# Kernel tuning notes

Hardware: AMD Instinct MI355X
Metric: run time of the kernel (lower is better)

Reference implementation:

```python
import jax, jax.numpy as jnp
import numpy as np

BN_EPS = 1e-5

def _batchnorm(x):
    # BatchNorm1d(affine=False) in training mode: per-feature batch stats, biased var
    mu = jnp.mean(x, axis=0, keepdims=True)
    var = jnp.mean((x - mu) ** 2, axis=0, keepdims=True)
    return (x - mu) / jnp.sqrt(var + BN_EPS)

def setup_inputs() -> dict:
    key = jax.random.key(0)
    ks = jax.random.split(key, 8)
    H, I, S, E = 1024, 4096, 128, 16384  # hidden, intermediate, sqrt(experts), experts
    std = 0.02
    return {
        "hidden_states": jax.random.normal(ks[0], (4, 2048, H), jnp.float32),
        "gate_proj_weight": jax.random.normal(ks[1], (I, H), jnp.float32) * std,
        "up_proj_weight": jax.random.normal(ks[2], (I, H), jnp.float32) * std,
        "down_proj_weight": jax.random.normal(ks[3], (H, I), jnp.float32) * std,
        "router_gate_x_weight": jax.random.normal(ks[4], (S, H), jnp.float32) * std,
        "router_gate_y_weight": jax.random.normal(ks[5], (S, H), jnp.float32) * std,
        "up_embed": jax.random.normal(ks[6], (E, H), jnp.float32) * std,
        "down_embed": jax.random.normal(ks[7], (E, H), jnp.float32) * std,
        "top_k": 16,
    }

def reference(hidden_states, gate_proj_weight, up_proj_weight, down_proj_weight,
              router_gate_x_weight, router_gate_y_weight, up_embed, down_embed, top_k):
    bsz, seq_len, H = hidden_states.shape
    x = hidden_states.reshape(-1, H)  # [T, H]
    S = router_gate_x_weight.shape[0]  # num_expert_sqrt

    # dual-axis router: two small gates -> batchnorm -> log-softmax
    lpx = jax.nn.log_softmax(_batchnorm(x @ router_gate_x_weight.T), axis=-1)  # [T, S]
    lpy = jax.nn.log_softmax(_batchnorm(x @ router_gate_y_weight.T), axis=-1)  # [T, S]
    # combined log-prob over S*S experts: expert (i,j) -> i*S + j
    combined = (lpx[:, :, None] + lpy[:, None, :]).reshape(-1, S * S)  # [T, S*S]
    scores, indices = jax.lax.top_k(combined, top_k)  # [T, K]
    routing_weights = jnp.exp(scores)  # [T, K] = p_x * p_y

    # embedding-based expert: gather up/down rows, dot-scale-combine
    ue = up_embed[indices]    # [T, K, H]
    de = down_embed[indices]  # [T, K, H]
    up_score = jnp.einsum('tkh,th->tk', ue, x)          # per-expert scalar
    experts_states = jnp.einsum('tk,tkh->th', routing_weights * up_score, de)

    # dense SwiGLU MLP branch
    mlp = (jax.nn.silu(x @ gate_proj_weight.T) * (x @ up_proj_weight.T)) @ down_proj_weight.T

    out = mlp + experts_states
    return out.reshape(bsz, seq_len, H)
```

## Files before the change

### kernel.cpp

```cpp
#include <hip/hip_runtime.h>
#include <hip/hip_bf16.h>
#include <math.h>

#define T_TOK 8192
#define HDIM  1024
#define IDIM  4096
#define SDIM  128
#define TOPK  16

typedef __bf16 bf16x8 __attribute__((ext_vector_type(8)));
typedef float  f32x4  __attribute__((ext_vector_type(4)));

__device__ __forceinline__ unsigned short f2bf(float f) {
    union { float f; unsigned u; } a; a.f = f;
    unsigned r = a.u + 0x7fffu + ((a.u >> 16) & 1u);
    return (unsigned short)(r >> 16);
}
__device__ __forceinline__ float bf2f(unsigned short b) {
    union { unsigned u; float f; } a; a.u = ((unsigned)b) << 16;
    return a.f;
}

__device__ __forceinline__ void gld_lds16(const void* g, void* l) {
    __builtin_amdgcn_global_load_lds(
        (__attribute__((address_space(1))) void*)g,
        (__attribute__((address_space(3))) void*)l,
        16, 0, 0);
}

struct CvtSegs {
    const float4* src[8];
    ushort4*      dst[8];
    int           end[8];
};

__global__ __launch_bounds__(256)
void cvt_all_kernel(CvtSegs segs) {
    int i = blockIdx.x * 256 + threadIdx.x;
    if (i >= segs.end[7]) return;
    int s = 0;
    #pragma unroll
    for (int k = 0; k < 7; ++k) s += (i >= segs.end[k]) ? 1 : 0;
    int base = (s == 0) ? 0 : segs.end[s - 1];
    int j = i - base;
    float4 v = segs.src[s][j];
    ushort4 o;
    o.x = f2bf(v.x); o.y = f2bf(v.y); o.z = f2bf(v.z); o.w = f2bf(v.w);
    segs.dst[s][j] = o;
}

template<int ADD>
__global__ __launch_bounds__(256)
void gemm_bt(const unsigned short* __restrict__ A, const unsigned short* __restrict__ B,
             float* __restrict__ C, int M, int N, int K) {
    __shared__ unsigned short As[4096];
    __shared__ unsigned short Bs[4096];
    const int tid  = threadIdx.x;
    const int lane = tid & 63;
    const int wave = tid >> 6;
    const int tm = blockIdx.x * 128;
    const int tn = blockIdx.y * 128;
    const int wm = (wave & 1) * 64;
    const int wn = (wave >> 1) * 64;
    const int quad = lane >> 4;
    const int tr   = lane & 15;

    f32x4 acc[4][4] = {};
    bf16x8 af[4], bfr[4];

    const int ua0 = tid,        am0 = ua0 & 127, ak0 = ua0 >> 7;
    const int ua1 = tid + 256,  am1 = ua1 & 127, ak1 = ua1 >> 7;

    auto issue = [&](int kt) {
        gld_lds16(A + (size_t)(tm + am0) * K + kt + ak0 * 8, &As[ua0 * 8]);
        gld_lds16(A + (size_t)(tm + am1) * K + kt + ak1 * 8, &As[ua1 * 8]);
        gld_lds16(B + (size_t)(tn + am0) * K + kt + ak0 * 8, &Bs[ua0 * 8]);
        gld_lds16(B + (size_t)(tn + am1) * K + kt + ak1 * 8, &Bs[ua1 * 8]);
    };
    auto rdfrags = [&]() {
        #pragma unroll
        for (int mi = 0; mi < 4; ++mi)
            af[mi] = *(const bf16x8*)&As[(quad * 128 + wm + mi * 16 + tr) * 8];
        #pragma unroll
        for (int ni = 0; ni < 4; ++ni)
            bfr[ni] = *(const bf16x8*)&Bs[(quad * 128 + wn + ni * 16 + tr) * 8];
    };
    auto mfmas = [&]() {
        #pragma unroll
        for (int mi = 0; mi < 4; ++mi)
            #pragma unroll
            for (int ni = 0; ni < 4; ++ni)
                acc[mi][ni] = __builtin_amdgcn_mfma_f32_16x16x32_bf16(af[mi], bfr[ni], acc[mi][ni], 0, 0, 0);
    };

    issue(0);
    asm volatile("s_waitcnt vmcnt(0)" ::: "memory");
    __syncthreads();
    rdfrags();
    for (int kt = 32; kt < K; kt += 32) {
        __syncthreads();
        issue(kt);
        mfmas();
        asm volatile("s_waitcnt vmcnt(0)" ::: "memory");
        __syncthreads();
        rdfrags();
    }
    mfmas();

    #pragma unroll
    for (int mi = 0; mi < 4; ++mi) {
        #pragma unroll
        for (int ni = 0; ni < 4; ++ni) {
            int col = tn + wn + ni * 16 + tr;
            #pragma unroll
            for (int r = 0; r < 4; ++r) {
                int row = tm + wm + mi * 16 + quad * 4 + r;
                size_t o = (size_t)row * N + col;
                float v = acc[mi][ni][r];
                if (ADD) v += C[o];
                C[o] = v;
            }
        }
    }
}

#define BARX() asm volatile("s_barrier" ::: "memory")
#define VMW4() asm volatile("s_waitcnt vmcnt(4)" ::: "memory")

#define RD_A(par, ks, MB) { const char* _p = lds + ((par) << 15) + ((ks) << 14); \
    af[0] = *(const bf16x8*)(_p + aoff[(MB)+0]); \
    af[1] = *(const bf16x8*)(_p + aoff[(MB)+1]); \
    af[2] = *(const bf16x8*)(_p + aoff[(MB)+2]); \
    af[3] = *(const bf16x8*)(_p + aoff[(MB)+3]); }

#define RD_B(par, ks) { const char* _p = lds + 65536 + ((par) << 15) + ((ks) << 14); \
    bfv[0] = *(const bf16x8*)(_p + boff[0]); \
    bfv[1] = *(const bf16x8*)(_p + boff[1]); \
    bfv[2] = *(const bf16x8*)(_p + boff[2]); \
    bfv[3] = *(const bf16x8*)(_p + boff[3]); }

#define MMA16(ACC) { __builtin_amdgcn_s_setprio(1); \
    _Pragma("unroll") \
    for (int _i = 0; _i < 4; ++_i) \
        _Pragma("unroll") \
        for (int _n = 0; _n < 4; ++_n) \
            ACC[_i][_n] = __builtin_amdgcn_mfma_f32_16x16x32_bf16(af[_i], bfv[_n], ACC[_i][_n], 0, 0, 0); \
    __builtin_amdgcn_s_setprio(0); }

__global__ __launch_bounds__(512, 2)
void gemm1_8ph(const unsigned short* __restrict__ Xb, const unsigned short* __restrict__ Wg,
               const unsigned short* __restrict__ Wu, unsigned short* __restrict__ Hb) {
    __shared__ __align__(16) char lds[131072];
    const int tid  = threadIdx.x;
    const int lane = tid & 63;
    const int wid  = tid >> 6;
    const int quad = lane >> 4;
    const int tr   = lane & 15;
    const int wm   = (wid >> 2) << 7;
    const int wn   = (wid & 3) << 6;

    const int bid = blockIdx.x;
    const int swz = (bid & 7) * 128 + (bid >> 3);
    const int gm  = (swz & 31) << 8;
    const int gn  = (swz >> 5) << 8;

    const int vsw  = (tid & 7) ^ ((tid >> 3) & 7);
    const int rowb = ((tid >> 3) << 1) | (vsw >> 2);
    const int cq8  = (vsw & 3) << 3;

    const unsigned short* pA0 = Xb + (size_t)(gm + rowb) * HDIM + cq8;
    const unsigned short* pA1 = pA0 + (size_t)128 * HDIM;
    auto wsrc = [&](int R) -> const unsigned short* {
        const unsigned short* base = ((R >> 4) & 1) ? Wu : Wg;
        int sr = ((R >> 5) << 4) | (R & 15);
        return base + (size_t)sr * HDIM + cq8;
    };
    const unsigned short* pB0 = wsrc(gn + rowb);
    const unsigned short* pB1 = wsrc(gn + rowb + 128);

    int aoff[8], boff[4];
    #pragma unroll
    for (int i = 0; i < 8; ++i) {
        int row = wm + i * 16 + tr;
        aoff[i] = ((row >> 1) << 7) | (((((row & 1) << 2) | quad) ^ ((row >> 1) & 7)) << 4);
    }
    #pragma unroll
    for (int i = 0; i < 4; ++i) {
        int row = wn + i * 16 + tr;
        boff[i] = ((row >> 1) << 7) | (((((row & 1) << 2) | quad) ^ ((row >> 1) & 7)) << 4);
    }

    f32x4 accL[4][4] = {};
    f32x4 accH[4][4] = {};
    bf16x8 af[4], bfv[4];

    auto stageA = [&](int nxt, int ks, int kOff) {
        char* d = lds + (nxt << 15) + (ks << 14) + (tid << 4);
        gld_lds16(pA0 + kOff, d);
        gld_lds16(pA1 + kOff, d + 8192);
    };
    auto stageB = [&](int nxt, int ks, int kOff) {
        char* d = lds + 65536 + (nxt << 15) + (ks << 14) + (tid << 4);
        gld_lds16(pB0 + kOff, d);
        gld_lds16(pB1 + kOff, d + 8192);
    };

    stageA(0, 0, 0);  stageB(0, 0, 0);
    stageA(0, 1, 32); stageB(0, 1, 32);
    asm volatile("s_waitcnt vmcnt(0)" ::: "memory");
    BARX();

    for (int t = 0; t < 16; ++t) {
        const int par = t & 1, nxt = par ^ 1;
        const int kN = (t < 15 ? t + 1 : 15) << 6;
        RD_A(par, 0, 0); RD_B(par, 0);
        stageA(nxt, 0, kN);
        BARX();
        MMA16(accL);
        BARX();
        RD_A(par, 0, 4);
        stageB(nxt, 0, kN);
        VMW4(); BARX();
        MMA16(accH);
        BARX();
        RD_A(par, 1, 0); RD_B(par, 1);
        stageA(nxt, 1, kN + 32);
        BARX();
        MMA16(accL);
        BARX();
        RD_A(par, 1, 4);
        stageB(nxt, 1, kN + 32);
        VMW4(); BARX();
        MMA16(accH);
        BARX();
    }
    asm volatile("s_waitcnt vmcnt(0)" ::: "memory");

    const size_t icb = (size_t)((gn + wn) >> 1) + tr;
    const int rbase = gm + wm + quad * 4;
    #pragma unroll
    for (int mi = 0; mi < 4; ++mi) {
        #pragma unroll
        for (int p = 0; p < 2; ++p) {
            #pragma unroll
            for (int r = 0; r < 4; ++r) {
                {
                    float g = accL[mi][2 * p][r], u = accL[mi][2 * p + 1][r];
                    float h = g / (1.0f + __expf(-g)) * u;
                    Hb[(size_t)(rbase + mi * 16 + r) * IDIM + icb + 16 * p] = f2bf(h);
                }
                {
                    float g = accH[mi][2 * p][r], u = accH[mi][2 * p + 1][r];
                    float h = g / (1.0f + __expf(-g)) * u;
                    Hb[(size_t)(rbase + 64 + mi * 16 + r) * IDIM + icb + 16 * p] = f2bf(h);
                }
            }
        }
    }
}

__global__ void bn_stats(const float* __restrict__ gxy, float* __restrict__ sums, float* __restrict__ ssq) {
    const int j = threadIdx.x;
    const int b = blockIdx.x;
    float s = 0.f, q = 0.f;
    for (int r = 0; r < 32; ++r) {
        float v = gxy[(size_t)(b * 32 + r) * 256 + j];
        s += v; q += v * v;
    }
    atomicAdd(&sums[j], s);
    atomicAdd(&ssq[j], q);
}

__global__ __launch_bounds__(256)
void routing_kernel(const float* __restrict__ gxy, const float* __restrict__ sums,
                    const float* __restrict__ ssq, int* __restrict__ oidx, float* __restrict__ owt) {
    const int lane = threadIdx.x & 63;
    const int t = blockIdx.x * 4 + (threadIdx.x >> 6);
    const float invT = 1.0f / (float)T_TOK;
    const float* g = gxy + (size_t)t * 256;

    float z[4];
    const int cols[4] = {lane, lane + 64, 128 + lane, 192 + lane};
    #pragma unroll
    for (int i = 0; i < 4; ++i) {
        int c = cols[i];
        float mu  = sums[c] * invT;
        float var = ssq[c] * invT - mu * mu;
        z[i] = (g[c] - mu) * rsqrtf(var + 1e-5f);
    }
    float mx = fmaxf(z[0], z[1]);
    float my = fmaxf(z[2], z[3]);
    #pragma unroll
    for (int m = 32; m >= 1; m >>= 1) {
        mx = fmaxf(mx, __shfl_xor(mx, m));
        my = fmaxf(my, __shfl_xor(my, m));
    }
    float sx = __expf(z[0] - mx) + __expf(z[1] - mx);
    float sy = __expf(z[2] - my) + __expf(z[3] - my);
    #pragma unroll
    for (int m = 32; m >= 1; m >>= 1) {
        sx += __shfl_xor(sx, m);
        sy += __shfl_xor(sy, m);
    }
    float lx0 = z[0] - (mx + __logf(sx)), lx1 = z[1] - (mx + __logf(sx));
    float ly0 = z[2] - (my + __logf(sy)), ly1 = z[3] - (my + __logf(sy));

    float aw = -INFINITY; int ai = 0;
    float bw = -INFINITY; int bi = 0;
    {
        float v0 = lx0, v1 = lx1;
        for (int i = 0; i < 16; ++i) {
            float v; int c;
            if (v0 >= v1) { v = v0; c = lane; } else { v = v1; c = lane + 64; }
            #pragma unroll
            for (int m = 32; m >= 1; m >>= 1) {
                float ov = __shfl_xor(v, m); int oc = __shfl_xor(c, m);
                if (ov > v || (ov == v && oc < c)) { v = ov; c = oc; }
            }
            if ((c & 63) == lane) { if (c < 64) v0 = -INFINITY; else v1 = -INFINITY; }
            if (lane == i) { aw = v; ai = c; }
        }
    }
    {
        float v0 = ly0, v1 = ly1;
        for (int i = 0; i < 16; ++i) {
            float v; int c;
            if (v0 >= v1) { v = v0; c = lane; } else { v = v1; c = lane + 64; }
            #pragma unroll
            for (int m = 32; m >= 1; m >>= 1) {
                float ov = __shfl_xor(v, m); int oc = __shfl_xor(c, m);
                if (ov > v || (ov == v && oc < c)) { v = ov; c = oc; }
            }
            if ((c & 63) == lane) { if (c < 64) v0 = -INFINITY; else v1 = -INFINITY; }
            if (lane == i) { bw = v; bi = c; }
        }
    }
    float cv[4];
    #pragma unroll
    for (int j = 0; j < 4; ++j) {
        int c = lane + 64 * j;
        cv[j] = __shfl(aw, c >> 4) + __shfl(bw, c & 15);
    }
    int myidx = 0; float myw = 0.f;
    for (int i = 0; i < 16; ++i) {
        float v = cv[0]; int c = lane;
        #pragma unroll
        for (int j = 1; j < 4; ++j) { int cc = lane + 64 * j; if (cv[j] > v) { v = cv[j]; c = cc; } }
        #pragma unroll
        for (int m = 32; m >= 1; m >>= 1) {
            float ov = __shfl_xor(v, m); int oc = __shfl_xor(c, m);
            if (ov > v || (ov == v && oc < c)) { v = ov; c = oc; }
        }
        #pragma unroll
        for (int j = 0; j < 4; ++j) if (c == lane + 64 * j) cv[j] = -INFINITY;
        int p = c >> 4, q = c & 15;
        int ex = __shfl(ai, p);
        int ey = __shfl(bi, q);
        if (lane == i) { myidx = ex * 128 + ey; myw = __expf(v); }
    }
    if (lane < 16) {
        oidx[t * TOPK + lane] = myidx;
        owt[t * TOPK + lane]  = myw;
    }
}

__global__ __launch_bounds__(256)
void expert_combine(const unsigned short* __restrict__ xb, const int* __restrict__ idx,
                    const float* __restrict__ wts, const unsigned short* __restrict__ ueb,
                    const unsigned short* __restrict__ deb, float* __restrict__ out) {
    const int t = blockIdx.x;
    const int tid = threadIdx.x;
    const int lane = tid & 63, wv = tid >> 6;
    __shared__ float part[TOPK * 4];
    __shared__ float sc[TOPK];
    ushort4 xv4 = ((const ushort4*)(xb + (size_t)t * HDIM))[tid];
    float x0 = bf2f(xv4.x), x1 = bf2f(xv4.y), x2 = bf2f(xv4.z), x3 = bf2f(xv4.w);
    int e[TOPK];
    #pragma unroll
    for (int k = 0; k < TOPK; ++k) e[k] = idx[t * TOPK + k];
    #pragma unroll
    for (int k = 0; k < TOPK; ++k) {
        ushort4 u4 = ((const ushort4*)(ueb + (size_t)e[k] * HDIM))[tid];
        float p = bf2f(u4.x) * x0 + bf2f(u4.y) * x1 + bf2f(u4.z) * x2 + bf2f(u4.w) * x3;
        #pragma unroll
        for (int m = 32; m >= 1; m >>= 1) p += __shfl_xor(p, m);
        if (lane == 0) part[k * 4 + wv] = p;
    }
    __syncthreads();
    if (tid < TOPK) {
        float s = part[tid * 4] + part[tid * 4 + 1] + part[tid * 4 + 2] + part[tid * 4 + 3];
        sc[tid] = s * wts[t * TOPK + tid];
    }
    __syncthreads();
    float4 acc = {0.f, 0.f, 0.f, 0.f};
    #pragma unroll
    for (int k = 0; k < TOPK; ++k) {
        float s = sc[k];
        ushort4 d4 = ((const ushort4*)(deb + (size_t)e[k] * HDIM))[tid];
        acc.x += s * bf2f(d4.x); acc.y += s * bf2f(d4.y);
        acc.z += s * bf2f(d4.z); acc.w += s * bf2f(d4.w);
    }
    ((float4*)(out + (size_t)t * HDIM))[tid] = acc;
}

extern "C" void kernel_launch(void* const* d_in, const int* in_sizes, int n_in,
                              void* d_out, int out_size, void* d_ws, size_t ws_size,
                              hipStream_t stream) {
    const float* x  = (const float*)d_in[0];
    const float* gw = (const float*)d_in[1];
    const float* uw = (const float*)d_in[2];
    const float* dw = (const float*)d_in[3];
    const float* wx = (const float*)d_in[4];
    const float* wy = (const float*)d_in[5];
    const float* ue = (const float*)d_in[6];
    const float* de = (const float*)d_in[7];
    float* out = (float*)d_out;

    char* ws = (char*)d_ws;
    size_t o = 0;
    auto alloc = [&](size_t bytes) { void* p = ws + o; o += (bytes + 255) & ~(size_t)255; return p; };
    unsigned short* xb    = (unsigned short*)alloc((size_t)T_TOK * HDIM * 2);
    unsigned short* gateb = (unsigned short*)alloc((size_t)IDIM * HDIM * 2);
    unsigned short* upb   = (unsigned short*)alloc((size_t)IDIM * HDIM * 2);
    unsigned short* downb = (unsigned short*)alloc((size_t)HDIM * IDIM * 2);
    unsigned short* wrb   = (unsigned short*)alloc((size_t)256 * HDIM * 2);
    unsigned short* ueb   = (unsigned short*)alloc((size_t)16384 * HDIM * 2);
    unsigned short* deb   = (unsigned short*)alloc((size_t)16384 * HDIM * 2);
    unsigned short* hbuf  = (unsigned short*)alloc((size_t)T_TOK * IDIM * 2);
    float* gxy  = (float*)alloc((size_t)T_TOK * 256 * 4);
    float* sums = (float*)alloc(256 * 4);
    float* ssq  = (float*)alloc(256 * 4);
    int*   idxs = (int*)alloc((size_t)T_TOK * TOPK * 4);
    float* wts  = (float*)alloc((size_t)T_TOK * TOPK * 4);

    CvtSegs segs;
    const float* srcs[8] = {x, gw, uw, dw, wx, wy, ue, de};
    unsigned short* dsts[8] = {xb, gateb, upb, downb, wrb, wrb + SDIM * HDIM, ueb, deb};
    const int cnt4[8] = {T_TOK * HDIM / 4, IDIM * HDIM / 4, IDIM * HDIM / 4, IDIM * HDIM / 4,
                         SDIM * HDIM / 4, SDIM * HDIM / 4, 16384 * HDIM / 4, 16384 * HDIM / 4};
    int acc = 0;
    for (int i = 0; i < 8; ++i) {
        segs.src[i] = (const float4*)srcs[i];
        segs.dst[i] = (ushort4*)dsts[i];
        acc += cnt4[i];
        segs.end[i] = acc;
    }
    cvt_all_kernel<<<(acc + 255) / 256, 256, 0, stream>>>(segs);

    hipMemsetAsync(sums, 0, 2 * 256 * 4, stream);
    gemm_bt<0><<<dim3(T_TOK / 128, 256 / 128), 256, 0, stream>>>(xb, wrb, gxy, T_TOK, 256, HDIM);
    bn_stats<<<256, 256, 0, stream>>>(gxy, sums, ssq);
    routing_kernel<<<T_TOK / 4, 256, 0, stream>>>(gxy, sums, ssq, idxs, wts);

    expert_combine<<<T_TOK, 256, 0, stream>>>(xb, idxs, wts, ueb, deb, out);

    gemm1_8ph<<<1024, 512, 0, stream>>>(xb, gateb, upb, hbuf);
    gemm_bt<1><<<dim3(T_TOK / 128, HDIM / 128), 256, 0, stream>>>(hbuf, downb, out, T_TOK, HDIM, IDIM);
}
```

Baseline: 740.8 us.

## Add dedicated 256x128-tile pipelined down-projection GEMM kernel

Replaces the generic 128x128 gemm_bt used for the down projection with a specialized kernel. It uses 512-thread blocks, 256x128 output tiles, double-buffered direct global-to-LDS loads with swizzled offsets, and an XCD-aware block swizzle over 256 blocks. The larger tile with 8x2 MFMA fragments per wave is meant to raise arithmetic intensity and overlap loads with MFMA, as gemm1_8ph already does. In exchange it uses more LDS per block (96KB) and a fixed grid of 256 blocks, which may underfill the device.

After: 690.4 us. -6.8%, faster.

```diff
diff --git a/kernel.cpp b/kernel.cpp
--- a/kernel.cpp
+++ b/kernel.cpp
@@ -126,6 +126,7 @@
 
 #define BARX() asm volatile("s_barrier" ::: "memory")
 #define VMW4() asm volatile("s_waitcnt vmcnt(4)" ::: "memory")
+#define VMW3() asm volatile("s_waitcnt vmcnt(3)" ::: "memory")
 
 #define RD_A(par, ks, MB) { const char* _p = lds + ((par) << 15) + ((ks) << 14); \
     af[0] = *(const bf16x8*)(_p + aoff[(MB)+0]); \
@@ -254,6 +255,109 @@
                     float h = g / (1.0f + __expf(-g)) * u;
                     Hb[(size_t)(rbase + 64 + mi * 16 + r) * IDIM + icb + 16 * p] = f2bf(h);
                 }
+            }
+        }
+    }
+}
+
+#define RD2_A(par, ks) { const char* _p = lds + ((par) << 15) + ((ks) << 14); \
+    _Pragma("unroll") \
+    for (int _i = 0; _i < 8; ++_i) af[_i] = *(const bf16x8*)(_p + aoff[_i]); }
+
+#define RD2_B(par, ks) { const char* _p = lds + 65536 + ((par) << 14) + ((ks) << 13); \
+    bfv[0] = *(const bf16x8*)(_p + boff[0]); \
+    bfv[1] = *(const bf16x8*)(_p + boff[1]); }
+
+#define MMA2() { __builtin_amdgcn_s_setprio(1); \
+    _Pragma("unroll") \
+    for (int _i = 0; _i < 8; ++_i) \
+        _Pragma("unroll") \
+        for (int _n = 0; _n < 2; ++_n) \
+            acc[_i][_n] = __builtin_amdgcn_mfma_f32_16x16x32_bf16(af[_i], bfv[_n], acc[_i][_n], 0, 0, 0); \
+    __builtin_amdgcn_s_setprio(0); }
+
+__global__ __launch_bounds__(512, 2)
+void gemm2_8ph(const unsigned short* __restrict__ A, const unsigned short* __restrict__ B,
+               float* __restrict__ C) {
+    __shared__ __align__(16) char lds[98304];
+    const int K = IDIM, N = HDIM;
+    const int tid  = threadIdx.x;
+    const int lane = tid & 63;
+    const int wid  = tid >> 6;
+    const int quad = lane >> 4;
+    const int tr   = lane & 15;
+    const int wm   = (wid >> 2) << 7;
+    const int wn   = (wid & 3) << 5;
+
+    const int bid = blockIdx.x;
+    const int swz = (bid & 7) * 32 + (bid >> 3);
+    const int gm  = (swz & 31) << 8;
+    const int gn  = (swz >> 5) << 7;
+
+    const int vsw  = (tid & 7) ^ ((tid >> 3) & 7);
+    const int rowb = ((tid >> 3) << 1) | (vsw >> 2);
+    const int cq8  = (vsw & 3) << 3;
+
+    const unsigned short* pA0 = A + (size_t)(gm + rowb) * K + cq8;
+    const unsigned short* pA1 = pA0 + (size_t)128 * K;
+    const unsigned short* pB0 = B + (size_t)(gn + rowb) * K + cq8;
+
+    int aoff[8], boff[2];
+    #pragma unroll
+    for (int i = 0; i < 8; ++i) {
+        int row = wm + i * 16 + tr;
+        aoff[i] = ((row >> 1) << 7) | (((((row & 1) << 2) | quad) ^ ((row >> 1) & 7)) << 4);
+    }
+    #pragma unroll
+    for (int i = 0; i < 2; ++i) {
+        int row = wn + i * 16 + tr;
+        boff[i] = ((row >> 1) << 7) | (((((row & 1) << 2) | quad) ^ ((row >> 1) & 7)) << 4);
+    }
+
+    f32x4 acc[8][2] = {};
+    bf16x8 af[8], bfv[2];
+
+    auto stageA = [&](int nxt, int ks, int kOff) {
+        char* d = lds + (nxt << 15) + (ks << 14) + (tid << 4);
+        gld_lds16(pA0 + kOff, d);
+        gld_lds16(pA1 + kOff, d + 8192);
+    };
+    auto stageB = [&](int nxt, int ks, int kOff) {
+        char* d = lds + 65536 + (nxt << 14) + (ks << 13) + (tid << 4);
+        gld_lds16(pB0 + kOff, d);
+    };
+
+    stageA(0, 0, 0); stageB(0, 0, 0);
+    stageA(0, 1, 32); stageB(0, 1, 32);
+    asm volatile("s_waitcnt vmcnt(0)" ::: "memory");
+    BARX();
+
+    for (int t = 0; t < 64; ++t) {
+        const int par = t & 1, nxt = par ^ 1;
+        const int kN = (t < 63 ? t + 1 : 63) << 6;
+        RD2_A(par, 0); RD2_B(par, 0);
+        stageA(nxt, 0, kN); stageB(nxt, 0, kN);
+        VMW3(); BARX();
+        MMA2();
+        BARX();
+        RD2_A(par, 1); RD2_B(par, 1);
+        stageA(nxt, 1, kN + 32); stageB(nxt, 1, kN + 32);
+        VMW3(); BARX();
+        MMA2();
+        BARX();
+    }
+    asm volatile("s_waitcnt vmcnt(0)" ::: "memory");
+
+    #pragma unroll
+    for (int mi = 0; mi < 8; ++mi) {
+        #pragma unroll
+        for (int ni = 0; ni < 2; ++ni) {
+            int col = gn + wn + ni * 16 + tr;
+            #pragma unroll
+            for (int r = 0; r < 4; ++r) {
+                int row = gm + wm + mi * 16 + quad * 4 + r;
+                size_t o = (size_t)row * N + col;
+                C[o] += acc[mi][ni][r];
             }
         }
     }
@@ -455,5 +559,5 @@
     expert_combine<<<T_TOK, 256, 0, stream>>>(xb, idxs, wts, ueb, deb, out);
 
     gemm1_8ph<<<1024, 512, 0, stream>>>(xb, gateb, upb, hbuf);
-    gemm_bt<1><<<dim3(T_TOK / 128, HDIM / 128), 256, 0, stream>>>(hbuf, downb, out, T_TOK, HDIM, IDIM);
-}
+    gemm2_8ph<<<256, 512, 0, stream>>>(hbuf, downb, out);
+}
```
